# Kernel tuning notes

Hardware: AMD Instinct MI355X
Metric: run time of the kernel (lower is better)

## Reference

```python
import jax, jax.numpy as jnp
import numpy as np

B, D, H, O = 4096, 1024, 8192, 1000

def _l2norm_rows(w):
    return w / jnp.maximum(jnp.linalg.norm(w, axis=1, keepdims=True), 1e-12)

def setup_inputs() -> dict:
    key = jax.random.key(0)
    k1, k2, k3 = jax.random.split(key, 3)
    x = jax.random.normal(k1, (B, D), dtype=jnp.float32)
    kohonen_weights = _l2norm_rows(jax.random.normal(k2, (H, D), dtype=jnp.float32))
    grossberg_weights = _l2norm_rows(jax.random.normal(k3, (O, H), dtype=jnp.float32))
    return {"x": x, "kohonen_weights": kohonen_weights, "grossberg_weights": grossberg_weights}

def reference(x, kohonen_weights, grossberg_weights):
    # x: [B, D] (already flat), kohonen_weights: [H, D], grossberg_weights: [O, H]
    x2 = jnp.sum(x * x, axis=1, keepdims=True)              # [B, 1]
    w2 = jnp.sum(kohonen_weights * kohonen_weights, axis=1)  # [H]
    # Euclidean cdist via the expanded quadratic form (same as torch.cdist p=2)
    sq = x2 + w2[None, :] - 2.0 * (x @ kohonen_weights.T)    # [B, H]
    distances = jnp.sqrt(jnp.maximum(sq, 0.0))
    winners = jnp.argmin(distances, axis=1)                  # [B] int
    # one_hot @ grossberg_weights.T is exactly a row gather of grossberg_weights.T
    output = jnp.take(grossberg_weights.T, winners, axis=0)  # [B, O]
    return (output, winners)
```

## Files before the change

kernel.cpp:

```cpp
#include <hip/hip_runtime.h>
#include <hip/hip_bf16.h>
#include <hip/hip_fp16.h>


#define BB 4096
#define DD 1024
#define HH 8192
#define OO 1000

#define BM 128
#define BN 128
#define BK 64
#define NTILES (HH / BN)

typedef _Float16 f16;
typedef float f32x4 __attribute__((ext_vector_type(4)));

typedef __attribute__((address_space(3))) uint32_t lds_u32_t;
typedef __attribute__((address_space(1))) uint32_t glb_u32_t;

__device__ __forceinline__ uint32_t packkey(float v, int col) {
  uint32_t u = __float_as_uint(v);
  uint32_t mask = (uint32_t)((int32_t)u >> 31) | 0x80000000u;
  u ^= mask;
  return (u & 0xFFFFFF80u) | (uint32_t)col;
}
__device__ __forceinline__ float unpackval(uint32_t k) {
  uint32_t u = k & 0xFFFFFF80u;
  uint32_t mask = (k & 0x80000000u) ? 0x80000000u : 0xFFFFFFFFu;
  return __uint_as_float(u ^ mask);
}
__device__ __forceinline__ void kmerge(uint32_t& k1, uint32_t& k2,
                                       uint32_t o1, uint32_t o2) {
  uint32_t mn = min(k1, o1);
  uint32_t alt = (k1 > o1) ? k2 : o2;
  k1 = max(k1, o1);
  k2 = max(mn, alt);
}

__global__ __launch_bounds__(256) void cvt_kernel(
    const float* __restrict__ x, const float* __restrict__ kw,
    uint8_t* __restrict__ xq, uint8_t* __restrict__ kq,
    const float* __restrict__ G, float* __restrict__ Gt) {
  const int tid = threadIdx.x;
  const int blk = blockIdx.x;
  __shared__ float tile[32][33];
  if (blk < (BB + HH) / 4) {
#pragma unroll
    for (int i = 0; i < 4; ++i) {
      int r = blk * 4 + i;
      const float* src = (r < BB) ? (x + (size_t)r * DD)
                                  : (kw + (size_t)(r - BB) * DD);
      uint8_t* dst = (r < BB) ? (xq + (size_t)r * DD)
                              : (kq + (size_t)(r - BB) * DD);
      float4 v = ((const float4*)src)[tid];
      int p = 0;
      p = __builtin_amdgcn_cvt_pk_fp8_f32(v.x, v.y, p, false);
      p = __builtin_amdgcn_cvt_pk_fp8_f32(v.z, v.w, p, true);
      ((int*)dst)[tid] = p;
    }
  } else {
    if (Gt == nullptr) return;
    const int tb = blk - (BB + HH) / 4;
    const int tx = tid & 31;
    const int ty = tid >> 5;
#pragma unroll 1
    for (int j4 = 0; j4 < 4; ++j4) {
      int tile_id = tb * 4 + j4;
      int h0 = (tile_id >> 5) * 32;
      int o0 = (tile_id & 31) * 32;
      __syncthreads();
#pragma unroll
      for (int j = 0; j < 4; ++j) {
        int o = o0 + ty + j * 8;
        if (o < OO) tile[ty + j * 8][tx] = G[(size_t)o * HH + h0 + tx];
      }
      __syncthreads();
#pragma unroll
      for (int j = 0; j < 4; ++j) {
        int o = o0 + tx;
        int h = h0 + ty + j * 8;
        if (o < OO) Gt[(size_t)h * OO + o] = tile[tx][ty + j * 8];
      }
    }
  }
}

__global__ __launch_bounds__(256) void gemm_top2(
    const uint8_t* __restrict__ A, const uint8_t* __restrict__ Bt,
    uint4* __restrict__ pk) {
  __shared__ __align__(16) uint8_t sA[BM * BK];
  __shared__ __align__(16) uint8_t sB[BN * BK];
  __shared__ uint2 mk[128][2];

  const int tid = threadIdx.x;
  const int w = tid >> 6;
  const int L = tid & 63;
  const int m0 = blockIdx.y * BM;
  const int n0 = blockIdx.x * BN;
  const int rm = (w >> 1) * 64;
  const int cn = (w & 1) * 64;

  f32x4 acc[4][4];
#pragma unroll
  for (int i = 0; i < 4; ++i)
#pragma unroll
    for (int j = 0; j < 4; ++j) {
      acc[i][j][0] = 0.f; acc[i][j][1] = 0.f; acc[i][j][2] = 0.f; acc[i][j][3] = 0.f;
    }

  const int lm = L & 15;
  const int lq = L >> 4;

  const int c0 = tid, c1 = tid + 256;
  const int r0 = c0 >> 2, r1 = c1 >> 2;
  const int s0 = ((c0 & 3) ^ ((r0 >> 1) & 3)) * 16;
  const int s1 = ((c1 & 3) ^ ((r1 >> 1) & 3)) * 16;
  const uint8_t* pA0 = A + (size_t)(m0 + r0) * DD + s0;
  const uint8_t* pA1 = A + (size_t)(m0 + r1) * DD + s1;
  const uint8_t* pB0 = Bt + (size_t)(n0 + r0) * DD + s0;
  const uint8_t* pB1 = Bt + (size_t)(n0 + r1) * DD + s1;

  const int t2 = (lm >> 1) & 3;
  const int raBase = (rm + lm) * BK;
  const int rbBase = (cn + lm) * BK;
  const int off0 = (((lq >> 1)) ^ t2) * 16 + (lq & 1) * 8;
  const int off1 = ((2 + (lq >> 1)) ^ t2) * 16 + (lq & 1) * 8;

  for (int kt = 0; kt < DD / BK; ++kt) {
    __syncthreads();
    __builtin_amdgcn_global_load_lds((const glb_u32_t*)pA0, (lds_u32_t*)(sA + c0 * 16), 16, 0, 0);
    __builtin_amdgcn_global_load_lds((const glb_u32_t*)pA1, (lds_u32_t*)(sA + c1 * 16), 16, 0, 0);
    __builtin_amdgcn_global_load_lds((const glb_u32_t*)pB0, (lds_u32_t*)(sB + c0 * 16), 16, 0, 0);
    __builtin_amdgcn_global_load_lds((const glb_u32_t*)pB1, (lds_u32_t*)(sB + c1 * 16), 16, 0, 0);
    pA0 += BK; pA1 += BK; pB0 += BK; pB1 += BK;
    __syncthreads();

    long long af[4], bf[4];
#pragma unroll
    for (int i = 0; i < 4; ++i)
      af[i] = *(const long long*)(sA + raBase + i * 16 * BK + off0);
#pragma unroll
    for (int j = 0; j < 4; ++j)
      bf[j] = *(const long long*)(sB + rbBase + j * 16 * BK + off0);
#pragma unroll
    for (int i = 0; i < 4; ++i)
#pragma unroll
      for (int j = 0; j < 4; ++j)
        acc[i][j] = __builtin_amdgcn_mfma_f32_16x16x32_fp8_fp8(af[i], bf[j], acc[i][j], 0, 0, 0);
#pragma unroll
    for (int i = 0; i < 4; ++i)
      af[i] = *(const long long*)(sA + raBase + i * 16 * BK + off1);
#pragma unroll
    for (int j = 0; j < 4; ++j)
      bf[j] = *(const long long*)(sB + rbBase + j * 16 * BK + off1);
#pragma unroll
    for (int i = 0; i < 4; ++i)
#pragma unroll
      for (int j = 0; j < 4; ++j)
        acc[i][j] = __builtin_amdgcn_mfma_f32_16x16x32_fp8_fp8(af[i], bf[j], acc[i][j], 0, 0, 0);
  }

  const int col0 = cn + lm;
#pragma unroll
  for (int i = 0; i < 4; ++i) {
#pragma unroll
    for (int r = 0; r < 4; ++r) {
      uint32_t k1 = 0, k2 = 0;
#pragma unroll
      for (int j = 0; j < 4; ++j) {
        uint32_t kj = packkey(acc[i][j][r], col0 + j * 16);
        if (kj > k1) { k2 = k1; k1 = kj; }
        else k2 = max(k2, kj);
      }
#pragma unroll
      for (int msk = 1; msk < 16; msk <<= 1) {
        uint32_t o1 = (uint32_t)__shfl_xor((int)k1, msk, 64);
        uint32_t o2 = (uint32_t)__shfl_xor((int)k2, msk, 64);
        kmerge(k1, k2, o1, o2);
      }
      if (lm == 0) {
        int rl = rm + i * 16 + lq * 4 + r;
        mk[rl][w & 1] = make_uint2(k1, k2);
      }
    }
  }
  __syncthreads();
  if (tid < 128) {
    uint2 a = mk[tid][0], b = mk[tid][1];
    pk[(size_t)(m0 + tid) * NTILES + blockIdx.x] = make_uint4(a.x, a.y, b.x, b.y);
  }
}

__global__ __launch_bounds__(256) void select_kernel(
    const float* __restrict__ x, const float* __restrict__ kw,
    const uint4* __restrict__ pk,
    const float* __restrict__ Gt, const float* __restrict__ G,
    float* __restrict__ out, float* __restrict__ out_w) {
  const int b = blockIdx.x * 4 + (threadIdx.x >> 6);
  const int L = threadIdx.x & 63;

  const float4* x4 = (const float4*)(x + (size_t)b * DD);
  float4 xv[4];
#pragma unroll
  for (int j = 0; j < 4; ++j) xv[j] = x4[L + 64 * j];

  uint4 kp = pk[(size_t)b * NTILES + L];

  double x2 = 0.0;
#pragma unroll
  for (int j = 0; j < 4; ++j)
    x2 += (double)xv[j].x * xv[j].x + (double)xv[j].y * xv[j].y +
          (double)xv[j].z * xv[j].z + (double)xv[j].w * xv[j].w;
#pragma unroll
  for (int msk = 1; msk < 64; msk <<= 1) x2 += __shfl_xor(x2, msk, 64);

  uint32_t m = max(kp.x, kp.z);
#pragma unroll
  for (int msk = 1; msk < 64; msk <<= 1)
    m = max(m, (uint32_t)__shfl_xor((int)m, msk, 64));
  const uint32_t thrk = packkey(unpackval(m) - 0.35f, 0);

  unsigned long long cand[4];
  cand[0] = __ballot(kp.x >= thrk);
  cand[1] = __ballot(kp.y >= thrk);
  cand[2] = __ballot(kp.z >= thrk);
  cand[3] = __ballot(kp.w >= thrk);

  double best = 1e300;
  int bestc = 0x7fffffff;
#pragma unroll 1
  for (int pass = 0; pass < 4; ++pass) {
    unsigned long long bits = cand[pass];
    uint32_t mykey = (pass == 0) ? kp.x : (pass == 1) ? kp.y
                    : (pass == 2) ? kp.z : kp.w;
    while (bits) {
      int tt = __ffsll((long long)bits) - 1;
      bits &= bits - 1;
      uint32_t kbt = (uint32_t)__shfl((int)mykey, tt, 64);
      int col = tt * 128 + (int)(kbt & 127u);
      const float4* k4 = (const float4*)(kw + (size_t)col * DD);
      double dot = 0.0, w2 = 0.0;
#pragma unroll
      for (int j = 0; j < 4; ++j) {
        float4 wv = k4[L + 64 * j];
        dot += (double)xv[j].x * wv.x + (double)xv[j].y * wv.y +
               (double)xv[j].z * wv.z + (double)xv[j].w * wv.w;
        w2 += (double)wv.x * wv.x + (double)wv.y * wv.y +
              (double)wv.z * wv.z + (double)wv.w * wv.w;
      }
#pragma unroll
      for (int msk = 1; msk < 64; msk <<= 1) {
        dot += __shfl_xor(dot, msk, 64);
        w2 += __shfl_xor(w2, msk, 64);
      }
      double sq = x2 + w2 - 2.0 * dot;
      if (sq < best || (sq == best && col < bestc)) { best = sq; bestc = col; }
    }
  }

  if (L == 0) out_w[b] = (float)bestc;
  if (Gt != nullptr) {
    const float4* gsrc = (const float4*)(Gt + (size_t)bestc * OO);
    float4* gdst = (float4*)(out + (size_t)b * OO);
#pragma unroll
    for (int j = 0; j < 4; ++j) {
      int q = L + 64 * j;
      if (q < OO / 4) gdst[q] = gsrc[q];
    }
  } else {
#pragma unroll 1
    for (int j = 0; j < 16; ++j) {
      int o = L + 64 * j;
      if (o < OO) out[(size_t)b * OO + o] = G[(size_t)o * HH + bestc];
    }
  }
}

extern "C" void kernel_launch(void* const* d_in, const int* in_sizes, int n_in,
                              void* d_out, int out_size, void* d_ws, size_t ws_size,
                              hipStream_t stream) {
  const float* x  = (const float*)d_in[0];
  const float* kw = (const float*)d_in[1];
  const float* gw = (const float*)d_in[2];
  float* out = (float*)d_out;
  float* out_w = out + (size_t)BB * OO;

  const size_t MB = 1024 * 1024;
  char* ws = (char*)d_ws;
  uint8_t* xq = (uint8_t*)(ws);
  uint8_t* kq = (uint8_t*)(ws + 4 * MB);
  uint4*   pk = (uint4*)(ws + 12 * MB);
  float*   Gt = (float*)(ws + 16 * MB);
  const size_t need = 16 * MB + sizeof(float) * (size_t)HH * OO;
  float* GtArg = (ws_size >= need) ? Gt : nullptr;

  int cvt_blocks = (BB + HH) / 4 + (GtArg ? 2048 : 0);
  cvt_kernel<<<cvt_blocks, 256, 0, stream>>>(x, kw, xq, kq, gw, GtArg);

  dim3 g(HH / BN, BB / BM);
  gemm_top2<<<g, 256, 0, stream>>>(xq, kq, pk);

  select_kernel<<<BB / 4, 256, 0, stream>>>(x, kw, pk, GtArg, gw, out, out_w);
}
```

Measured before the change: 219.3 us.

## Use 16x16x128 scaled FP8 MFMA with BK=128 and wider swizzled LDS tiles

Replaces the pair of 16x16x32 fp8 MFMAs per K step with the gfx950 scaled 16x16x128 f8f6f4 MFMA, using unit scales (0x7F exponent). The K tile grows to 128, which halves the number of K iterations and barrier pairs. Each lane now issues four global-to-LDS loads per matrix, and the XOR swizzle is widened to 8 chunks so that 128-bit LDS fragment reads avoid bank conflicts. LDS usage per tile doubles, which may reduce occupancy.

```diff
diff --git a/kernel.cpp b/kernel.cpp
--- a/kernel.cpp
+++ b/kernel.cpp
@@ -10,11 +10,14 @@
 
 #define BM 128
 #define BN 128
-#define BK 64
+#define BK 128
 #define NTILES (HH / BN)
 
 typedef _Float16 f16;
 typedef float f32x4 __attribute__((ext_vector_type(4)));
+typedef int v8i __attribute__((ext_vector_type(8)));
+typedef int v4i __attribute__((ext_vector_type(4)));
+union Frag { v8i v; v4i h[2]; };
 
 typedef __attribute__((address_space(3))) uint32_t lds_u32_t;
 typedef __attribute__((address_space(1))) uint32_t glb_u32_t;
@@ -112,53 +115,57 @@
   const int lm = L & 15;
   const int lq = L >> 4;
 
-  const int c0 = tid, c1 = tid + 256;
-  const int r0 = c0 >> 2, r1 = c1 >> 2;
-  const int s0 = ((c0 & 3) ^ ((r0 >> 1) & 3)) * 16;
-  const int s1 = ((c1 & 3) ^ ((r1 >> 1) & 3)) * 16;
-  const uint8_t* pA0 = A + (size_t)(m0 + r0) * DD + s0;
-  const uint8_t* pA1 = A + (size_t)(m0 + r1) * DD + s1;
-  const uint8_t* pB0 = Bt + (size_t)(n0 + r0) * DD + s0;
-  const uint8_t* pB1 = Bt + (size_t)(n0 + r1) * DD + s1;
-
-  const int t2 = (lm >> 1) & 3;
+  const uint8_t* pA[4];
+  const uint8_t* pB[4];
+  int dst[4];
+#pragma unroll
+  for (int j = 0; j < 4; ++j) {
+    int c = tid + 256 * j;
+    int r = c >> 3;
+    int so = ((c & 7) ^ (r & 7)) * 16;
+    pA[j] = A + (size_t)(m0 + r) * DD + so;
+    pB[j] = Bt + (size_t)(n0 + r) * DD + so;
+    dst[j] = c * 16;
+  }
+
+  const int s = lm & 7;
+  const int o_lo = ((2 * lq) ^ s) * 16;
+  const int o_hi = ((2 * lq + 1) ^ s) * 16;
   const int raBase = (rm + lm) * BK;
   const int rbBase = (cn + lm) * BK;
-  const int off0 = (((lq >> 1)) ^ t2) * 16 + (lq & 1) * 8;
-  const int off1 = ((2 + (lq >> 1)) ^ t2) * 16 + (lq & 1) * 8;
 
   for (int kt = 0; kt < DD / BK; ++kt) {
     __syncthreads();
-    __builtin_amdgcn_global_load_lds((const glb_u32_t*)pA0, (lds_u32_t*)(sA + c0 * 16), 16, 0, 0);
-    __builtin_amdgcn_global_load_lds((const glb_u32_t*)pA1, (lds_u32_t*)(sA + c1 * 16), 16, 0, 0);
-    __builtin_amdgcn_global_load_lds((const glb_u32_t*)pB0, (lds_u32_t*)(sB + c0 * 16), 16, 0, 0);
-    __builtin_amdgcn_global_load_lds((const glb_u32_t*)pB1, (lds_u32_t*)(sB + c1 * 16), 16, 0, 0);
-    pA0 += BK; pA1 += BK; pB0 += BK; pB1 += BK;
+#pragma unroll
+    for (int j = 0; j < 4; ++j) {
+      __builtin_amdgcn_global_load_lds((const glb_u32_t*)pA[j], (lds_u32_t*)(sA + dst[j]), 16, 0, 0);
+      __builtin_amdgcn_global_load_lds((const glb_u32_t*)pB[j], (lds_u32_t*)(sB + dst[j]), 16, 0, 0);
+      pA[j] += BK; pB[j] += BK;
+    }
     __syncthreads();
 
-    long long af[4], bf[4];
+    Frag af[4], bf[4];
+#pragma unroll
+    for (int i = 0; i < 4; ++i) {
+      const uint8_t* base = sA + raBase + i * 16 * BK;
+      af[i].h[0] = *(const v4i*)(base + o_lo);
+      af[i].h[1] = *(const v4i*)(base + o_hi);
+    }
+#pragma unroll
+    for (int j = 0; j < 4; ++j) {
+      const uint8_t* base = sB + rbBase + j * 16 * BK;
+      bf[j].h[0] = *(const v4i*)(base + o_lo);
+      bf[j].h[1] = *(const v4i*)(base + o_hi);
+    }
 #pragma unroll
     for (int i = 0; i < 4; ++i)
-      af[i] = *(const long long*)(sA + raBase + i * 16 * BK + off0);
-#pragma unroll
-    for (int j = 0; j < 4; ++j)
-      bf[j] = *(const long long*)(sB + rbBase + j * 16 * BK + off0);
-#pragma unroll
-    for (int i = 0; i < 4; ++i)
 #pragma unroll
       for (int j = 0; j < 4; ++j)
-        acc[i][j] = __builtin_amdgcn_mfma_f32_16x16x32_fp8_fp8(af[i], bf[j], acc[i][j], 0, 0, 0);
-#pragma unroll
-    for (int i = 0; i < 4; ++i)
-      af[i] = *(const long long*)(sA + raBase + i * 16 * BK + off1);
-#pragma unroll
-    for (int j = 0; j < 4; ++j)
-      bf[j] = *(const long long*)(sB + rbBase + j * 16 * BK + off1);
-#pragma unroll
-    for (int i = 0; i < 4; ++i)
-#pragma unroll
-      for (int j = 0; j < 4; ++j)
-        acc[i][j] = __builtin_amdgcn_mfma_f32_16x16x32_fp8_fp8(af[i], bf[j], acc[i][j], 0, 0, 0);
+        acc[i][j] = __builtin_amdgcn_mfma_scale_f32_16x16x128_f8f6f4(
+            af[i].v, bf[j].v, acc[i][j],
+            0 , 0 ,
+            0, 0x7F7F7F7Fu ,
+            0, 0x7F7F7F7Fu );
   }
 
   const int col0 = cn + lm;
```

New measurement: 247.1 us. 12.7% more time.

## Enlarge GEMM M tile to 256 and swizzle block order for L2 reuse

Applied to the files above, without the earlier changes.

Doubles the block tile height from 128 to 256 rows, so each wave computes a 128x64 sub-tile with 32 accumulators. This raises arithmetic intensity per LDS load and halves redundant B-tile fetches. It also remaps the linear block id so groups of 8 consecutive blocks share column tiles for better L2 locality, and sets launch bounds of 2 blocks per CU. The cost is higher register pressure, which could cause spills or lower occupancy, and the host grid must match the new BM.

```diff
diff --git a/kernel.cpp b/kernel.cpp
--- a/kernel.cpp
+++ b/kernel.cpp
@@ -8,7 +8,7 @@
 #define HH 8192
 #define OO 1000
 
-#define BM 128
+#define BM 256
 #define BN 128
 #define BK 64
 #define NTILES (HH / BN)
@@ -86,24 +86,31 @@
   }
 }
 
-__global__ __launch_bounds__(256) void gemm_top2(
+__global__ __launch_bounds__(256, 2) void gemm_top2(
     const uint8_t* __restrict__ A, const uint8_t* __restrict__ Bt,
     uint4* __restrict__ pk) {
   __shared__ __align__(16) uint8_t sA[BM * BK];
   __shared__ __align__(16) uint8_t sB[BN * BK];
-  __shared__ uint2 mk[128][2];
+  __shared__ uint2 mk[BM][2];
 
   const int tid = threadIdx.x;
   const int w = tid >> 6;
   const int L = tid & 63;
-  const int m0 = blockIdx.y * BM;
-  const int n0 = blockIdx.x * BN;
-  const int rm = (w >> 1) * 64;
-  const int cn = (w & 1) * 64;
-
-  f32x4 acc[4][4];
-#pragma unroll
-  for (int i = 0; i < 4; ++i)
+
+  const int bid = blockIdx.y * gridDim.x + blockIdx.x;
+  const int c8 = bid & 7;
+  const int tt = bid >> 3;
+  const int nx = c8 * 8 + (tt & 7);
+  const int my = tt >> 3;
+  const int m0 = my * BM;
+  const int n0 = nx * BN;
+
+  const int wr = w >> 1;
+  const int wc = w & 1;
+
+  f32x4 acc[8][4];
+#pragma unroll
+  for (int i = 0; i < 8; ++i)
 #pragma unroll
     for (int j = 0; j < 4; ++j) {
       acc[i][j][0] = 0.f; acc[i][j][1] = 0.f; acc[i][j][2] = 0.f; acc[i][j][3] = 0.f;
@@ -112,58 +119,73 @@
   const int lm = L & 15;
   const int lq = L >> 4;
 
-  const int c0 = tid, c1 = tid + 256;
-  const int r0 = c0 >> 2, r1 = c1 >> 2;
-  const int s0 = ((c0 & 3) ^ ((r0 >> 1) & 3)) * 16;
-  const int s1 = ((c1 & 3) ^ ((r1 >> 1) & 3)) * 16;
-  const uint8_t* pA0 = A + (size_t)(m0 + r0) * DD + s0;
-  const uint8_t* pA1 = A + (size_t)(m0 + r1) * DD + s1;
-  const uint8_t* pB0 = Bt + (size_t)(n0 + r0) * DD + s0;
-  const uint8_t* pB1 = Bt + (size_t)(n0 + r1) * DD + s1;
+  const uint8_t* pA[4]; int dA[4];
+#pragma unroll
+  for (int j = 0; j < 4; ++j) {
+    int c = tid + 256 * j;
+    int r = c >> 2;
+    int so = ((c & 3) ^ ((r >> 1) & 3)) * 16;
+    pA[j] = A + (size_t)(m0 + r) * DD + so;
+    dA[j] = c * 16;
+  }
+  const uint8_t* pB[2]; int dB[2];
+#pragma unroll
+  for (int j = 0; j < 2; ++j) {
+    int c = tid + 256 * j;
+    int r = c >> 2;
+    int so = ((c & 3) ^ ((r >> 1) & 3)) * 16;
+    pB[j] = Bt + (size_t)(n0 + r) * DD + so;
+    dB[j] = c * 16;
+  }
 
   const int t2 = (lm >> 1) & 3;
-  const int raBase = (rm + lm) * BK;
-  const int rbBase = (cn + lm) * BK;
+  const int raBase = (wr * 128 + lm) * BK;
+  const int rbBase = (wc * 64 + lm) * BK;
   const int off0 = (((lq >> 1)) ^ t2) * 16 + (lq & 1) * 8;
   const int off1 = ((2 + (lq >> 1)) ^ t2) * 16 + (lq & 1) * 8;
 
   for (int kt = 0; kt < DD / BK; ++kt) {
     __syncthreads();
-    __builtin_amdgcn_global_load_lds((const glb_u32_t*)pA0, (lds_u32_t*)(sA + c0 * 16), 16, 0, 0);
-    __builtin_amdgcn_global_load_lds((const glb_u32_t*)pA1, (lds_u32_t*)(sA + c1 * 16), 16, 0, 0);
-    __builtin_amdgcn_global_load_lds((const glb_u32_t*)pB0, (lds_u32_t*)(sB + c0 * 16), 16, 0, 0);
-    __builtin_amdgcn_global_load_lds((const glb_u32_t*)pB1, (lds_u32_t*)(sB + c1 * 16), 16, 0, 0);
-    pA0 += BK; pA1 += BK; pB0 += BK; pB1 += BK;
+#pragma unroll
+    for (int j = 0; j < 4; ++j) {
+      __builtin_amdgcn_global_load_lds((const glb_u32_t*)pA[j], (lds_u32_t*)(sA + dA[j]), 16, 0, 0);
+      pA[j] += BK;
+    }
+#pragma unroll
+    for (int j = 0; j < 2; ++j) {
+      __builtin_amdgcn_global_load_lds((const glb_u32_t*)pB[j], (lds_u32_t*)(sB + dB[j]), 16, 0, 0);
+      pB[j] += BK;
+    }
     __syncthreads();
 
-    long long af[4], bf[4];
-#pragma unroll
-    for (int i = 0; i < 4; ++i)
+    long long af[8], bf[4];
+#pragma unroll
+    for (int i = 0; i < 8; ++i)
       af[i] = *(const long long*)(sA + raBase + i * 16 * BK + off0);
 #pragma unroll
     for (int j = 0; j < 4; ++j)
       bf[j] = *(const long long*)(sB + rbBase + j * 16 * BK + off0);
 #pragma unroll
-    for (int i = 0; i < 4; ++i)
+    for (int i = 0; i < 8; ++i)
 #pragma unroll
       for (int j = 0; j < 4; ++j)
         acc[i][j] = __builtin_amdgcn_mfma_f32_16x16x32_fp8_fp8(af[i], bf[j], acc[i][j], 0, 0, 0);
 #pragma unroll
-    for (int i = 0; i < 4; ++i)
+    for (int i = 0; i < 8; ++i)
       af[i] = *(const long long*)(sA + raBase + i * 16 * BK + off1);
 #pragma unroll
     for (int j = 0; j < 4; ++j)
       bf[j] = *(const long long*)(sB + rbBase + j * 16 * BK + off1);
 #pragma unroll
-    for (int i = 0; i < 4; ++i)
+    for (int i = 0; i < 8; ++i)
 #pragma unroll
       for (int j = 0; j < 4; ++j)
         acc[i][j] = __builtin_amdgcn_mfma_f32_16x16x32_fp8_fp8(af[i], bf[j], acc[i][j], 0, 0, 0);
   }
 
-  const int col0 = cn + lm;
-#pragma unroll
-  for (int i = 0; i < 4; ++i) {
+  const int col0 = wc * 64 + lm;
+#pragma unroll
+  for (int i = 0; i < 8; ++i) {
 #pragma unroll
     for (int r = 0; r < 4; ++r) {
       uint32_t k1 = 0, k2 = 0;
@@ -180,15 +202,15 @@
         kmerge(k1, k2, o1, o2);
       }
       if (lm == 0) {
-        int rl = rm + i * 16 + lq * 4 + r;
-        mk[rl][w & 1] = make_uint2(k1, k2);
+        int rl = wr * 128 + i * 16 + lq * 4 + r;
+        mk[rl][wc] = make_uint2(k1, k2);
       }
     }
   }
   __syncthreads();
-  if (tid < 128) {
+  {
     uint2 a = mk[tid][0], b = mk[tid][1];
-    pk[(size_t)(m0 + tid) * NTILES + blockIdx.x] = make_uint4(a.x, a.y, b.x, b.y);
+    pk[(size_t)(m0 + tid) * NTILES + nx] = make_uint4(a.x, a.y, b.x, b.y);
   }
 }
 
```

Result: no change. 218.9 us (-0.2%).
